# Performance work log

Measured on AMD Instinct MI355X. Metric: run time of the kernel, lower is better.

Reference implementation:

```python
import jax, jax.numpy as jnp
import numpy as np

B, NP, NS = 64, 32, 72
H, F = 4, 64
HD = H * F            # 256
CS, CE = 7, 16
L = 4
NC = 110
EPS = 1e-6


def setup_inputs() -> dict:
    key = jax.random.key(0)
    ks = jax.random.split(key, 32)
    def n(k, shape, s=0.05):
        return (jax.random.normal(k, shape, jnp.float32) * s)
    spatial_obs = jax.random.normal(ks[0], (B, NP, NS), jnp.float32)
    card_context = jax.random.normal(ks[1], (B, CS, CE), jnp.float32)
    adj = (jax.random.uniform(ks[2], (NS, NS)) > 0.85).astype(jnp.float32)
    adj = jnp.maximum(adj, jnp.eye(NS, dtype=jnp.float32))  # self-loops
    return {
        'spatial_obs': spatial_obs,
        'card_context': card_context,
        'adj': adj,
        'ctx_W': n(ks[3], (CS * CE, HD)), 'ctx_b': jnp.zeros((HD,)),
        'lnc_s': jnp.ones((HD,)), 'lnc_b': jnp.zeros((HD,)),
        'in_W': n(ks[4], (NP, HD)), 'in_b': jnp.zeros((HD,)),
        'lnp_s': jnp.ones((L, HD)), 'lnp_b': jnp.zeros((L, HD)),
        'cp_W': n(ks[5], (L, HD, HD)), 'cp_b': jnp.zeros((L, HD)),
        'Wl': n(ks[6], (L, HD, HD)), 'Wr': n(ks[7], (L, HD, HD)),
        'Wa': n(ks[8], (L, H, F)),
        'op_W': n(ks[9], (L, HD, HD)), 'op_b': jnp.zeros((L, HD)),
        'card_W': n(ks[10], (HD, NC)), 'card_b': jnp.zeros((NC,)),
        'at_W': n(ks[11], (HD, 3)), 'at_b': jnp.zeros((3,)),
        'src_W': n(ks[12], (HD, NS)), 'src_b': jnp.zeros((NS,)),
        'tgt_W': n(ks[13], (HD, NS)), 'tgt_b': jnp.zeros((NS,)),
        'v1_W': n(ks[14], (HD, 128)), 'v1_b': jnp.zeros((128,)),
        'v2_W': n(ks[15], (128, 1)), 'v2_b': jnp.zeros((1,)),
    }


def _layernorm(x, s, b):
    m = jnp.mean(x, axis=-1, keepdims=True)
    v = jnp.var(x, axis=-1, keepdims=True)
    return (x - m) * jax.lax.rsqrt(v + EPS) * s + b


def _gatv2(h, adj, Wl, Wr, Wa):
    # h: (B, N, HD); GATv2: e_ij = Wa . LeakyReLU(Wl h_i + Wr h_j)
    b, n, _ = h.shape
    hl = jnp.einsum('bnd,de->bne', h, Wl).reshape(b, n, H, F)
    hr = jnp.einsum('bnd,de->bne', h, Wr).reshape(b, n, H, F)
    e = jax.nn.leaky_relu(hl[:, :, None, :, :] + hr[:, None, :, :, :], 0.2)  # (B,N,N,H,F)
    scores = jnp.einsum('bijhf,hf->bijh', e, Wa)
    scores = jnp.where(adj[None, :, :, None] > 0, scores, -1e9)
    attn = jax.nn.softmax(scores, axis=2)  # softmax over neighbors j
    out = jnp.einsum('bijh,bjhf->bihf', attn, hr)
    return out.reshape(b, n, HD)


def reference(spatial_obs, card_context, adj,
              ctx_W, ctx_b, lnc_s, lnc_b, in_W, in_b,
              lnp_s, lnp_b, cp_W, cp_b, Wl, Wr, Wa, op_W, op_b,
              card_W, card_b, at_W, at_b, src_W, src_b, tgt_W, tgt_b,
              v1_W, v1_b, v2_W, v2_b):
    b = spatial_obs.shape[0]
    ctx = card_context.reshape(b, CS * CE)
    g = jax.nn.relu(_layernorm(ctx @ ctx_W + ctx_b, lnc_s, lnc_b))  # (B, HD)
    x = jnp.einsum('bps,pd->bsd', spatial_obs, in_W) + in_b          # (B, NS, HD)
    for l in range(L):
        h = _layernorm(x, lnp_s[l], lnp_b[l])
        h = h + (g @ cp_W[l] + cp_b[l])[:, None, :]
        hg = _gatv2(h, adj, Wl[l], Wr[l], Wa[l])
        x = x + (hg @ op_W[l] + op_b[l])
    ge = jnp.mean(x, axis=1)  # (B, HD)
    card_logits = ge @ card_W + card_b
    action_type_logits = ge @ at_W + at_b
    src_logits = ge @ src_W + src_b
    tgt_logits = ge @ tgt_W + tgt_b
    value = jnp.tanh(jax.nn.relu(ge @ v1_W + v1_b) @ v2_W + v2_b)
    return (card_logits, action_type_logits, src_logits, tgt_logits, value)
```

## Files before the change

### kernel.cpp

```cpp
#include <hip/hip_runtime.h>
#include <hip/hip_bf16.h>
#include <math.h>

#define B 64
#define NP 32
#define NS 72
#define NH 4
#define NF 64
#define HD 256
#define CTXD 112
#define NL 4
#define NC 110
#define LN_EPS 1e-6f
#define TI 8
#define GROWS 8

typedef __hip_bfloat16 bf16;

__device__ __forceinline__ float ldv(const float* p, int i) { return p[i]; }
__device__ __forceinline__ float ldv(const bf16* p, int i) { return __bfloat162float(p[i]); }
__device__ __forceinline__ void stv(float* p, int i, float v) { p[i] = v; }
__device__ __forceinline__ void stv(bf16* p, int i, float v) { p[i] = __float2bfloat16(v); }

__global__ void k_detect(const void* adj, int* flag) {
  if (threadIdx.x == 0 && blockIdx.x == 0) {
    *flag = (((const unsigned short*)adj)[0] == 0x3F80u) ? 1 : 0;
  }
}

__device__ __forceinline__ void block_reduce_2(float& a, float& b, float* sred, int t) {
  #pragma unroll
  for (int o = 32; o > 0; o >>= 1) { a += __shfl_down(a, o); b += __shfl_down(b, o); }
  if ((t & 63) == 0) { sred[(t >> 6) * 2] = a; sred[(t >> 6) * 2 + 1] = b; }
  __syncthreads();
  a = sred[0] + sred[2] + sred[4] + sred[6];
  b = sred[1] + sred[3] + sred[5] + sred[7];
}

template <typename T>
__device__ void ctx_body(const T* cardctx, const T* ctxW, const T* ctxb,
                         const T* lncs, const T* lncb, float* g,
                         float* sred, float* sctx) {
  int b = blockIdx.x, t = threadIdx.x;
  if (t < CTXD) sctx[t] = ldv(cardctx, b * CTXD + t);
  __syncthreads();
  float acc = ldv(ctxb, t);
  for (int k = 0; k < CTXD; ++k) acc += sctx[k] * ldv(ctxW, k * HD + t);
  float a = acc, bb = acc * acc;
  block_reduce_2(a, bb, sred, t);
  float mean = a * (1.f / HD);
  float var = bb * (1.f / HD) - mean * mean;
  float r = rsqrtf(var + LN_EPS);
  float v = (acc - mean) * r * ldv(lncs, t) + ldv(lncb, t);
  g[b * HD + t] = fmaxf(v, 0.f);
}
__global__ void __launch_bounds__(256) k_ctx(const void* cardctx, const void* ctxW, const void* ctxb,
                      const void* lncs, const void* lncb, float* g, const int* flag) {
  __shared__ float sred[8];
  __shared__ float sctx[CTXD];
  if (*flag) ctx_body<bf16>((const bf16*)cardctx, (const bf16*)ctxW, (const bf16*)ctxb,
                            (const bf16*)lncs, (const bf16*)lncb, g, sred, sctx);
  else ctx_body<float>((const float*)cardctx, (const float*)ctxW, (const float*)ctxb,
                       (const float*)lncs, (const float*)lncb, g, sred, sctx);
}

template <typename T>
__device__ void inproj_body(const T* spat, const T* inW, const T* inb, float* x, float* ssp) {
  int blk = blockIdx.x; int b = blk / NS; int s = blk % NS; int t = threadIdx.x;
  if (t < NP) ssp[t] = ldv(spat, (b * NP + t) * NS + s);
  __syncthreads();
  float acc = ldv(inb, t);
  #pragma unroll 8
  for (int p = 0; p < NP; ++p) acc += ssp[p] * ldv(inW, p * HD + t);
  x[blk * HD + t] = acc;
}
__global__ void __launch_bounds__(256) k_inproj(const void* spat, const void* inW, const void* inb,
                         float* x, const int* flag) {
  __shared__ float ssp[NP];
  if (*flag) inproj_body<bf16>((const bf16*)spat, (const bf16*)inW, (const bf16*)inb, x, ssp);
  else inproj_body<float>((const float*)spat, (const float*)inW, (const float*)inb, x, ssp);
}

template <typename T>
__device__ void cproj_body(const float* g, const T* cpW, const T* cpb, float* c, int l, float* sg) {
  int b = blockIdx.x, t = threadIdx.x;
  sg[t] = g[b * HD + t];
  __syncthreads();
  const T* W = cpW + l * HD * HD;
  float acc = ldv(cpb, l * HD + t);
  for (int k = 0; k < HD; ++k) acc += sg[k] * ldv(W, k * HD + t);
  c[b * HD + t] = acc;
}
__global__ void __launch_bounds__(256) k_cproj(const float* g, const void* cpW, const void* cpb,
                        float* c, int l, const int* flag) {
  __shared__ float sg[HD];
  if (*flag) cproj_body<bf16>(g, (const bf16*)cpW, (const bf16*)cpb, c, l, sg);
  else cproj_body<float>(g, (const float*)cpW, (const float*)cpb, c, l, sg);
}

template <typename T>
__device__ void lnadd_body(const float* x, const float* c, const T* lnps, const T* lnpb,
                           float* h, int l, float* sred) {
  int row = blockIdx.x, t = threadIdx.x;
  float v = x[row * HD + t];
  float a = v, bb = v * v;
  block_reduce_2(a, bb, sred, t);
  float mean = a * (1.f / HD);
  float var = bb * (1.f / HD) - mean * mean;
  float r = rsqrtf(var + LN_EPS);
  float o = (v - mean) * r * ldv(lnps, l * HD + t) + ldv(lnpb, l * HD + t)
          + c[(row / NS) * HD + t];
  h[row * HD + t] = o;
}
__global__ void __launch_bounds__(256) k_lnadd(const float* x, const float* c, const void* lnps, const void* lnpb,
                        float* h, int l, const int* flag) {
  __shared__ float sred[8];
  if (*flag) lnadd_body<bf16>(x, c, (const bf16*)lnps, (const bf16*)lnpb, h, l, sred);
  else lnadd_body<float>(x, c, (const float*)lnps, (const float*)lnpb, h, l, sred);
}

template <typename T>
__device__ void gemmlr_body(const float* h, const T* Wl, const T* Wr, float* hl, float* hr,
                            int l, float (*xs)[HD]) {
  int row0 = blockIdx.x * GROWS; int t = threadIdx.x;
  #pragma unroll
  for (int r = 0; r < GROWS; ++r) xs[r][t] = h[(row0 + r) * HD + t];
  __syncthreads();
  const T* Wlp = Wl + l * HD * HD;
  const T* Wrp = Wr + l * HD * HD;
  float acc[GROWS];
  #pragma unroll
  for (int r = 0; r < GROWS; ++r) acc[r] = 0.f;
  for (int k = 0; k < HD; ++k) {
    float w = ldv(Wlp, k * HD + t);
    #pragma unroll
    for (int r = 0; r < GROWS; ++r) acc[r] += xs[r][k] * w;
  }
  #pragma unroll
  for (int r = 0; r < GROWS; ++r) hl[(row0 + r) * HD + t] = acc[r];
  #pragma unroll
  for (int r = 0; r < GROWS; ++r) acc[r] = 0.f;
  for (int k = 0; k < HD; ++k) {
    float w = ldv(Wrp, k * HD + t);
    #pragma unroll
    for (int r = 0; r < GROWS; ++r) acc[r] += xs[r][k] * w;
  }
  #pragma unroll
  for (int r = 0; r < GROWS; ++r) hr[(row0 + r) * HD + t] = acc[r];
}
__global__ void __launch_bounds__(256) k_gemm_lr(const float* h, const void* Wl, const void* Wr,
                          float* hl, float* hr, int l, const int* flag) {
  __shared__ float xs[GROWS][HD];
  if (*flag) gemmlr_body<bf16>(h, (const bf16*)Wl, (const bf16*)Wr, hl, hr, l, xs);
  else gemmlr_body<float>(h, (const float*)Wl, (const float*)Wr, hl, hr, l, xs);
}

template <typename T>
__device__ void gat_body(const float* hl, const float* hr, const T* adj, const T* Wa,
                         float* hg, int l, float (*shl)[HD], float* swa,
                         float (*ssc)[NH][NS]) {
  int blk = blockIdx.x; int b = blk / (NS / TI); int i0 = (blk % (NS / TI)) * TI;
  int t = threadIdx.x;
  swa[t] = ldv(Wa, l * HD + t);
  #pragma unroll
  for (int r = 0; r < TI; ++r) shl[r][t] = hl[(b * NS + i0 + r) * HD + t];
  __syncthreads();
  for (int p = t; p < TI * NH * NS; p += 256) {
    int j = p % NS; int hh = (p / NS) % NH; int r = p / (NS * NH);
    const float* hrp = hr + (b * NS + j) * HD + hh * NF;
    const float* hlp = &shl[r][hh * NF];
    const float* wap = &swa[hh * NF];
    float sum = 0.f;
    #pragma unroll 8
    for (int f = 0; f < NF; ++f) {
      float e = hlp[f] + hrp[f];
      e = (e > 0.f) ? e : 0.2f * e;
      sum += e * wap[f];
    }
    ssc[r][hh][j] = sum;
  }
  __syncthreads();
  int wid = t >> 6, lane = t & 63;
  for (int task = wid; task < TI * NH; task += 4) {
    int r = task >> 2; int hh = task & 3;
    int i = i0 + r;
    float a1 = ldv(adj, i * NS + lane);
    float s1 = (a1 > 0.f) ? ssc[r][hh][lane] : -1e30f;
    float s2 = -1e30f;
    if (lane < NS - 64) {
      float a2 = ldv(adj, i * NS + 64 + lane);
      if (a2 > 0.f) s2 = ssc[r][hh][64 + lane];
    }
    float m = fmaxf(s1, s2);
    #pragma unroll
    for (int o = 32; o > 0; o >>= 1) m = fmaxf(m, __shfl_xor(m, o));
    float e1 = (s1 > -1e29f) ? __expf(s1 - m) : 0.f;
    float e2 = (s2 > -1e29f) ? __expf(s2 - m) : 0.f;
    float se = e1 + e2;
    #pragma unroll
    for (int o = 32; o > 0; o >>= 1) se += __shfl_xor(se, o);
    float inv = 1.f / se;
    ssc[r][hh][lane] = e1 * inv;
    if (lane < NS - 64) ssc[r][hh][64 + lane] = e2 * inv;
  }
  __syncthreads();
  int hh = t >> 6;
  float acc[TI];
  #pragma unroll
  for (int r = 0; r < TI; ++r) acc[r] = 0.f;
  for (int j = 0; j < NS; ++j) {
    float hv = hr[(b * NS + j) * HD + t];
    #pragma unroll
    for (int r = 0; r < TI; ++r) acc[r] += ssc[r][hh][j] * hv;
  }
  #pragma unroll
  for (int r = 0; r < TI; ++r) hg[(b * NS + i0 + r) * HD + t] = acc[r];
}
__global__ void __launch_bounds__(256) k_gat(const float* hl, const float* hr, const void* adj, const void* Wa,
                      float* hg, int l, const int* flag) {
  __shared__ float shl[TI][HD];
  __shared__ float swa[HD];
  __shared__ float ssc[TI][NH][NS];
  if (*flag) gat_body<bf16>(hl, hr, (const bf16*)adj, (const bf16*)Wa, hg, l, shl, swa, ssc);
  else gat_body<float>(hl, hr, (const float*)adj, (const float*)Wa, hg, l, shl, swa, ssc);
}

template <typename T>
__device__ void gemmop_body(const float* hg, const T* opW, const T* opb, float* x,
                            int l, float (*xs)[HD]) {
  int row0 = blockIdx.x * GROWS; int t = threadIdx.x;
  #pragma unroll
  for (int r = 0; r < GROWS; ++r) xs[r][t] = hg[(row0 + r) * HD + t];
  __syncthreads();
  const T* W = opW + l * HD * HD;
  float acc[GROWS];
  #pragma unroll
  for (int r = 0; r < GROWS; ++r) acc[r] = 0.f;
  for (int k = 0; k < HD; ++k) {
    float w = ldv(W, k * HD + t);
    #pragma unroll
    for (int r = 0; r < GROWS; ++r) acc[r] += xs[r][k] * w;
  }
  float bias = ldv(opb, l * HD + t);
  #pragma unroll
  for (int r = 0; r < GROWS; ++r) x[(row0 + r) * HD + t] += acc[r] + bias;
}
__global__ void __launch_bounds__(256) k_gemm_op(const float* hg, const void* opW, const void* opb,
                          float* x, int l, const int* flag) {
  __shared__ float xs[GROWS][HD];
  if (*flag) gemmop_body<bf16>(hg, (const bf16*)opW, (const bf16*)opb, x, l, xs);
  else gemmop_body<float>(hg, (const float*)opW, (const float*)opb, x, l, xs);
}

template <typename T>
__device__ void heads_body(const float* x,
                           const T* cardW, const T* cardb, const T* atW, const T* atb,
                           const T* srcW, const T* srcb, const T* tgtW, const T* tgtb,
                           const T* v1W, const T* v1b, const T* v2W, const T* v2b,
                           T* out, float* sge, float* sh1) {
  int b = blockIdx.x, t = threadIdx.x;
  float acc = 0.f;
  for (int s = 0; s < NS; ++s) acc += x[(b * NS + s) * HD + t];
  sge[t] = acc * (1.f / NS);
  __syncthreads();
  for (int p = t; p < NC + 3 + NS + NS; p += 256) {
    if (p < NC) {
      int col = p;
      float o = ldv(cardb, col);
      for (int k = 0; k < HD; ++k) o += sge[k] * ldv(cardW, k * NC + col);
      stv(out, b * NC + col, o);
    } else if (p < NC + 3) {
      int col = p - NC;
      float o = ldv(atb, col);
      for (int k = 0; k < HD; ++k) o += sge[k] * ldv(atW, k * 3 + col);
      stv(out, B * NC + b * 3 + col, o);
    } else if (p < NC + 3 + NS) {
      int col = p - NC - 3;
      float o = ldv(srcb, col);
      for (int k = 0; k < HD; ++k) o += sge[k] * ldv(srcW, k * NS + col);
      stv(out, B * NC + B * 3 + b * NS + col, o);
    } else {
      int col = p - NC - 3 - NS;
      float o = ldv(tgtb, col);
      for (int k = 0; k < HD; ++k) o += sge[k] * ldv(tgtW, k * NS + col);
      stv(out, B * NC + B * 3 + B * NS + b * NS + col, o);
    }
  }
  if (t < 128) {
    float o = ldv(v1b, t);
    for (int k = 0; k < HD; ++k) o += sge[k] * ldv(v1W, k * 128 + t);
    sh1[t] = fmaxf(o, 0.f);
  }
  __syncthreads();
  if (t < 64) {
    float pv = sh1[t] * ldv(v2W, t) + sh1[t + 64] * ldv(v2W, t + 64);
    #pragma unroll
    for (int o = 32; o > 0; o >>= 1) pv += __shfl_xor(pv, o);
    if (t == 0) stv(out, B * (NC + 3 + NS + NS) + b, tanhf(pv + ldv(v2b, 0)));
  }
}
__global__ void __launch_bounds__(256) k_heads(const float* x,
                        const void* cardW, const void* cardb, const void* atW, const void* atb,
                        const void* srcW, const void* srcb, const void* tgtW, const void* tgtb,
                        const void* v1W, const void* v1b, const void* v2W, const void* v2b,
                        void* out, const int* flag) {
  __shared__ float sge[HD];
  __shared__ float sh1[128];
  if (*flag) heads_body<bf16>(x, (const bf16*)cardW, (const bf16*)cardb, (const bf16*)atW,
                              (const bf16*)atb, (const bf16*)srcW, (const bf16*)srcb,
                              (const bf16*)tgtW, (const bf16*)tgtb, (const bf16*)v1W,
                              (const bf16*)v1b, (const bf16*)v2W, (const bf16*)v2b,
                              (bf16*)out, sge, sh1);
  else heads_body<float>(x, (const float*)cardW, (const float*)cardb, (const float*)atW,
                         (const float*)atb, (const float*)srcW, (const float*)srcb,
                         (const float*)tgtW, (const float*)tgtb, (const float*)v1W,
                         (const float*)v1b, (const float*)v2W, (const float*)v2b,
                         (float*)out, sge, sh1);
}

extern "C" void kernel_launch(void* const* d_in, const int* in_sizes, int n_in,
                              void* d_out, int out_size, void* d_ws, size_t ws_size,
                              hipStream_t stream) {
  const void* spatial = d_in[0];
  const void* cardctx = d_in[1];
  const void* adj = d_in[2];
  const void* ctxW = d_in[3]; const void* ctxb = d_in[4];
  const void* lncs = d_in[5]; const void* lncb = d_in[6];
  const void* inW = d_in[7];  const void* inb = d_in[8];
  const void* lnps = d_in[9]; const void* lnpb = d_in[10];
  const void* cpW = d_in[11]; const void* cpb = d_in[12];
  const void* Wl = d_in[13];  const void* Wr = d_in[14]; const void* Wa = d_in[15];
  const void* opW = d_in[16]; const void* opb = d_in[17];
  const void* cardW = d_in[18]; const void* cardb = d_in[19];
  const void* atW = d_in[20];   const void* atb = d_in[21];
  const void* srcW = d_in[22];  const void* srcb = d_in[23];
  const void* tgtW = d_in[24];  const void* tgtb = d_in[25];
  const void* v1W = d_in[26];   const void* v1b = d_in[27];
  const void* v2W = d_in[28];   const void* v2b = d_in[29];

  int* flag = (int*)d_ws;
  float* base = (float*)((char*)d_ws + 256);
  float* g  = base;
  float* c  = g + B * HD;
  float* x  = c + B * HD;
  float* h  = x + B * NS * HD;
  float* hl = h + B * NS * HD;
  float* hr = hl + B * NS * HD;
  float* hg = h;

  k_detect<<<1, 64, 0, stream>>>(adj, flag);
  k_ctx<<<B, HD, 0, stream>>>(cardctx, ctxW, ctxb, lncs, lncb, g, flag);
  k_inproj<<<B * NS, HD, 0, stream>>>(spatial, inW, inb, x, flag);
  for (int l = 0; l < NL; ++l) {
    k_cproj<<<B, HD, 0, stream>>>(g, cpW, cpb, c, l, flag);
    k_lnadd<<<B * NS, HD, 0, stream>>>(x, c, lnps, lnpb, h, l, flag);
    k_gemm_lr<<<B * NS / GROWS, HD, 0, stream>>>(h, Wl, Wr, hl, hr, l, flag);
    k_gat<<<B * (NS / TI), HD, 0, stream>>>(hl, hr, adj, Wa, hg, l, flag);
    k_gemm_op<<<B * NS / GROWS, HD, 0, stream>>>(hg, opW, opb, x, l, flag);
  }
  k_heads<<<B, HD, 0, stream>>>(x, cardW, cardb, atW, atb, srcW, srcb, tgtW, tgtb,
                                v1W, v1b, v2W, v2b, d_out, flag);
}
```

Baseline: 789.7 us.

## Restructure GATv2 kernel per batch-head with abs-form LeakyReLU and register-resident hr

The GAT kernel now launches one block per (batch, head) instead of per (batch, 8-row tile). It rewrites LeakyReLU(x) as 0.6x+0.4|x|, so the linear part splits into per-i and per-j dot products and the inner loop becomes abs plus FMA. Each lane keeps its neighbour j's hr slice in registers, and hl/hr and a transposed attention matrix are staged in padded shared memory for the aggregation step. The aim is to cut redundant global hr reads and per-element ALU work, at the cost of heavy register use (launch_bounds 256,1), fewer blocks (256), and slightly different floating-point rounding.

```diff
diff --git a/kernel.cpp b/kernel.cpp
--- a/kernel.cpp
+++ b/kernel.cpp
@@ -12,8 +12,10 @@
 #define NL 4
 #define NC 110
 #define LN_EPS 1e-6f
-#define TI 8
 #define GROWS 8
+
+#define SH 68
+#define SA 76
 
 typedef __hip_bfloat16 bf16;
 
@@ -156,73 +158,119 @@
 }
 
 template <typename T>
-__device__ void gat_body(const float* hl, const float* hr, const T* adj, const T* Wa,
-                         float* hg, int l, float (*shl)[HD], float* swa,
-                         float (*ssc)[NH][NS]) {
-  int blk = blockIdx.x; int b = blk / (NS / TI); int i0 = (blk % (NS / TI)) * TI;
-  int t = threadIdx.x;
-  swa[t] = ldv(Wa, l * HD + t);
-  #pragma unroll
-  for (int r = 0; r < TI; ++r) shl[r][t] = hl[(b * NS + i0 + r) * HD + t];
-  __syncthreads();
-  for (int p = t; p < TI * NH * NS; p += 256) {
-    int j = p % NS; int hh = (p / NS) % NH; int r = p / (NS * NH);
-    const float* hrp = hr + (b * NS + j) * HD + hh * NF;
-    const float* hlp = &shl[r][hh * NF];
-    const float* wap = &swa[hh * NF];
-    float sum = 0.f;
-    #pragma unroll 8
-    for (int f = 0; f < NF; ++f) {
-      float e = hlp[f] + hrp[f];
-      e = (e > 0.f) ? e : 0.2f * e;
-      sum += e * wap[f];
+__device__ void gat_body(const float* __restrict__ hl, const float* __restrict__ hr,
+                         const T* __restrict__ adj, const T* __restrict__ Wa,
+                         float* __restrict__ hg, int l,
+                         float* hl_s, float* hr_s, float* attnT, float* wa04_s) {
+  const int bid = blockIdx.x;
+  const int b = bid >> 2, hh = bid & 3;
+  const int t = threadIdx.x;
+  const int w = t >> 6, L = t & 63;
+
+  const float* hlbase = hl + (size_t)(b * NS) * HD + hh * NF;
+  const float* hrbase = hr + (size_t)(b * NS) * HD + hh * NF;
+
+  const float4* hrg1 = (const float4*)(hrbase + L * HD);
+  const float4* hrg2 = (const float4*)(hrbase + (64 + (L & 7)) * HD);
+  float4 hr1[16], hr2[16];
+  #pragma unroll
+  for (int q = 0; q < 16; ++q) hr1[q] = hrg1[q];
+  #pragma unroll
+  for (int q = 0; q < 16; ++q) hr2[q] = hrg2[q];
+
+  if (t < NF) wa04_s[t] = 0.4f * ldv(Wa, l * HD + hh * NF + t);
+
+  const float4* hlg4 = (const float4*)hlbase;
+  const float4* hrg4 = (const float4*)hrbase;
+  for (int c = t; c < NS * 16; c += 256) {
+    int j = c >> 4, q = c & 15;
+    *(float4*)&hl_s[j * SH + 4 * q] = hlg4[j * 64 + q];
+    *(float4*)&hr_s[j * SH + 4 * q] = hrg4[j * 64 + q];
+  }
+  __syncthreads();
+
+  float B1 = 0.f, B2 = 0.f;
+  #pragma unroll
+  for (int q = 0; q < 16; ++q) {
+    float4 w4 = *(const float4*)&wa04_s[4 * q];
+    B1 = fmaf(w4.x, hr1[q].x, B1); B1 = fmaf(w4.y, hr1[q].y, B1);
+    B1 = fmaf(w4.z, hr1[q].z, B1); B1 = fmaf(w4.w, hr1[q].w, B1);
+    B2 = fmaf(w4.x, hr2[q].x, B2); B2 = fmaf(w4.y, hr2[q].y, B2);
+    B2 = fmaf(w4.z, hr2[q].z, B2); B2 = fmaf(w4.w, hr2[q].w, B2);
+  }
+  float B15_1 = 1.5f * B1, B15_2 = 1.5f * B2;
+  float wa04L = wa04_s[L];
+
+  for (int p = 0; p < 18; ++p) {
+    int i = w + 4 * p;
+    float av = wa04L * hl_s[i * SH + L];
+    #pragma unroll
+    for (int o = 32; o > 0; o >>= 1) av += __shfl_xor(av, o);
+    float A15 = 1.5f * av;
+
+    float acc1 = 0.f, acc2 = 0.f;
+    #pragma unroll
+    for (int q = 0; q < 16; ++q) {
+      float4 h4 = *(const float4*)&hl_s[i * SH + 4 * q];
+      float4 w4 = *(const float4*)&wa04_s[4 * q];
+      float e;
+      e = h4.x + hr1[q].x; acc1 = fmaf(w4.x, fabsf(e), acc1);
+      e = h4.y + hr1[q].y; acc1 = fmaf(w4.y, fabsf(e), acc1);
+      e = h4.z + hr1[q].z; acc1 = fmaf(w4.z, fabsf(e), acc1);
+      e = h4.w + hr1[q].w; acc1 = fmaf(w4.w, fabsf(e), acc1);
+      e = h4.x + hr2[q].x; acc2 = fmaf(w4.x, fabsf(e), acc2);
+      e = h4.y + hr2[q].y; acc2 = fmaf(w4.y, fabsf(e), acc2);
+      e = h4.z + hr2[q].z; acc2 = fmaf(w4.z, fabsf(e), acc2);
+      e = h4.w + hr2[q].w; acc2 = fmaf(w4.w, fabsf(e), acc2);
     }
-    ssc[r][hh][j] = sum;
-  }
-  __syncthreads();
-  int wid = t >> 6, lane = t & 63;
-  for (int task = wid; task < TI * NH; task += 4) {
-    int r = task >> 2; int hh = task & 3;
-    int i = i0 + r;
-    float a1 = ldv(adj, i * NS + lane);
-    float s1 = (a1 > 0.f) ? ssc[r][hh][lane] : -1e30f;
-    float s2 = -1e30f;
-    if (lane < NS - 64) {
-      float a2 = ldv(adj, i * NS + 64 + lane);
-      if (a2 > 0.f) s2 = ssc[r][hh][64 + lane];
+    float s1 = A15 + B15_1 + acc1;
+    float s2 = A15 + B15_2 + acc2;
+    float a1 = ldv(adj, i * NS + L);
+    s1 = (a1 > 0.f) ? s1 : -1e30f;
+    if (L < 8) {
+      float a2 = ldv(adj, i * NS + 64 + L);
+      s2 = (a2 > 0.f) ? s2 : -1e30f;
+    } else {
+      s2 = -1e30f;
     }
     float m = fmaxf(s1, s2);
     #pragma unroll
     for (int o = 32; o > 0; o >>= 1) m = fmaxf(m, __shfl_xor(m, o));
-    float e1 = (s1 > -1e29f) ? __expf(s1 - m) : 0.f;
-    float e2 = (s2 > -1e29f) ? __expf(s2 - m) : 0.f;
+    float e1 = __expf(s1 - m);
+    float e2 = __expf(s2 - m);
     float se = e1 + e2;
     #pragma unroll
     for (int o = 32; o > 0; o >>= 1) se += __shfl_xor(se, o);
     float inv = 1.f / se;
-    ssc[r][hh][lane] = e1 * inv;
-    if (lane < NS - 64) ssc[r][hh][64 + lane] = e2 * inv;
-  }
-  __syncthreads();
-  int hh = t >> 6;
-  float acc[TI];
-  #pragma unroll
-  for (int r = 0; r < TI; ++r) acc[r] = 0.f;
-  for (int j = 0; j < NS; ++j) {
-    float hv = hr[(b * NS + j) * HD + t];
-    #pragma unroll
-    for (int r = 0; r < TI; ++r) acc[r] += ssc[r][hh][j] * hv;
-  }
-  #pragma unroll
-  for (int r = 0; r < TI; ++r) hg[(b * NS + i0 + r) * HD + t] = acc[r];
-}
-__global__ void __launch_bounds__(256) k_gat(const float* hl, const float* hr, const void* adj, const void* Wa,
+    attnT[L * SA + i] = e1 * inv;
+    if (L < 8) attnT[(64 + L) * SA + i] = e2 * inv;
+  }
+  __syncthreads();
+
+  for (int p = 0; p < 5; ++p) {
+    int g = w + 4 * p;
+    if (g >= 18) break;
+    int i0 = 4 * g;
+    float a0 = 0.f, a1 = 0.f, a2 = 0.f, a3 = 0.f;
+    #pragma unroll 4
+    for (int j = 0; j < NS; ++j) {
+      float4 at = *(const float4*)&attnT[j * SA + i0];
+      float hv = hr_s[j * SH + L];
+      a0 = fmaf(at.x, hv, a0); a1 = fmaf(at.y, hv, a1);
+      a2 = fmaf(at.z, hv, a2); a3 = fmaf(at.w, hv, a3);
+    }
+    float* o = hg + (size_t)(b * NS + i0) * HD + hh * NF + L;
+    o[0] = a0; o[HD] = a1; o[2 * HD] = a2; o[3 * HD] = a3;
+  }
+}
+__global__ void __launch_bounds__(256, 1) k_gat(const float* hl, const float* hr, const void* adj, const void* Wa,
                       float* hg, int l, const int* flag) {
-  __shared__ float shl[TI][HD];
-  __shared__ float swa[HD];
-  __shared__ float ssc[TI][NH][NS];
-  if (*flag) gat_body<bf16>(hl, hr, (const bf16*)adj, (const bf16*)Wa, hg, l, shl, swa, ssc);
-  else gat_body<float>(hl, hr, (const float*)adj, (const float*)Wa, hg, l, shl, swa, ssc);
+  __shared__ float hl_s[NS * SH];
+  __shared__ float hr_s[NS * SH];
+  __shared__ float attnT[NS * SA];
+  __shared__ float wa04_s[NF];
+  if (*flag) gat_body<bf16>(hl, hr, (const bf16*)adj, (const bf16*)Wa, hg, l, hl_s, hr_s, attnT, wa04_s);
+  else gat_body<float>(hl, hr, (const float*)adj, (const float*)Wa, hg, l, hl_s, hr_s, attnT, wa04_s);
 }
 
 template <typename T>
@@ -355,7 +403,7 @@
     k_cproj<<<B, HD, 0, stream>>>(g, cpW, cpb, c, l, flag);
     k_lnadd<<<B * NS, HD, 0, stream>>>(x, c, lnps, lnpb, h, l, flag);
     k_gemm_lr<<<B * NS / GROWS, HD, 0, stream>>>(h, Wl, Wr, hl, hr, l, flag);
-    k_gat<<<B * (NS / TI), HD, 0, stream>>>(hl, hr, adj, Wa, hg, l, flag);
+    k_gat<<<B * NH, 256, 0, stream>>>(hl, hr, adj, Wa, hg, l, flag);
     k_gemm_op<<<B * NS / GROWS, HD, 0, stream>>>(hg, opW, opb, x, l, flag);
   }
   k_heads<<<B, HD, 0, stream>>>(x, cardW, cardb, atW, atb, srcW, srcb, tgtW, tgtb,
```

Result: faster. 652.7 us (-17.4%).
